# Optimization experiments

Hardware: AMD Instinct MI355X
Metric: run time of the kernel (lower is better)

The kernel has to match this reference:

```python
import jax, jax.numpy as jnp
import numpy as np

DIM = 768
HEADS = 12
HEAD_DIM = DIM // HEADS
HIDDEN = int(DIM * 4.0)


def setup_inputs() -> dict:
    key = jax.random.key(0)
    ks = jax.random.split(key, 12)
    s = lambda *shape: 0.02
    inp = {
        "x": jax.random.normal(ks[0], (8, 1024, DIM), dtype=jnp.float32),
        "norm1_g": jnp.ones((DIM,), jnp.float32),
        "norm1_b": jnp.zeros((DIM,), jnp.float32),
        "qkv_w": jax.random.normal(ks[1], (DIM, 3 * DIM), jnp.float32) * 0.02,
        "qkv_b": jnp.zeros((3 * DIM,), jnp.float32),
        "proj_w": jax.random.normal(ks[2], (DIM, DIM), jnp.float32) * 0.02,
        "proj_b": jnp.zeros((DIM,), jnp.float32),
        "norm2_g": jnp.ones((DIM,), jnp.float32),
        "norm2_b": jnp.zeros((DIM,), jnp.float32),
        "fc1_w": jax.random.normal(ks[3], (DIM, HIDDEN), jnp.float32) * 0.02,
        "fc1_b": jnp.zeros((HIDDEN,), jnp.float32),
        "fc2_w": jax.random.normal(ks[4], (HIDDEN, DIM), jnp.float32) * 0.02,
        "fc2_b": jnp.zeros((DIM,), jnp.float32),
    }
    return inp


def _layernorm(x, g, b, eps=1e-5):
    mu = jnp.mean(x, axis=-1, keepdims=True)
    var = jnp.mean(jnp.square(x - mu), axis=-1, keepdims=True)
    return (x - mu) * jax.lax.rsqrt(var + eps) * g + b


def _attention(x, qkv_w, qkv_b, proj_w, proj_b):
    B, N, C = x.shape
    qkv = x @ qkv_w + qkv_b                      # [B, N, 3C]
    qkv = qkv.reshape(B, N, 3, HEADS, HEAD_DIM)
    q, k, v = jnp.moveaxis(qkv, 2, 0)            # each [B, N, H, D]
    scale = HEAD_DIM ** -0.5
    scores = jnp.einsum("bnhd,bmhd->bhnm", q, k) * scale  # [B, H, N, N]
    attn = jax.nn.softmax(scores, axis=-1)
    out = jnp.einsum("bhnm,bmhd->bnhd", attn, v).reshape(B, N, C)
    return out @ proj_w + proj_b


def reference(x, norm1_g, norm1_b, qkv_w, qkv_b, proj_w, proj_b,
              norm2_g, norm2_b, fc1_w, fc1_b, fc2_w, fc2_b):
    # Pre-norm transformer block (inference: DropPath = identity)
    x = x + _attention(_layernorm(x, norm1_g, norm1_b), qkv_w, qkv_b, proj_w, proj_b)
    h = _layernorm(x, norm2_g, norm2_b)
    h = jax.nn.gelu(h @ fc1_w + fc1_b, approximate=False) @ fc2_w + fc2_b
    return x + h
```

## Files before the change

### kernel.cpp

```cpp
#include <hip/hip_runtime.h>

typedef __attribute__((ext_vector_type(8))) short s16x8;
typedef __attribute__((ext_vector_type(4))) short s16x4;
typedef __attribute__((ext_vector_type(4))) float f32x4;

static __device__ __forceinline__ short f2bf(float f) {
    unsigned u = __builtin_bit_cast(unsigned, f);
    u = (u + 0x7FFFu + ((u >> 16) & 1u)) >> 16;
    return (short)u;
}

__device__ __forceinline__ void gload16(const short* g, short* l) {
    __builtin_amdgcn_global_load_lds(
        (const __attribute__((address_space(1))) void*)g,
        (__attribute__((address_space(3))) void*)l,
        16, 0, 0);
}

__global__ __launch_bounds__(256) void transpose_convert(
    const float* __restrict__ W, short* __restrict__ Wt, int K, int N)
{
    __shared__ float tile[32][33];
    const int bx = blockIdx.x * 32;
    const int by = blockIdx.y * 32;
    const int tx = threadIdx.x;
    const int ty = threadIdx.y;
    for (int i = 0; i < 32; i += 8)
        tile[ty + i][tx] = W[(size_t)(by + ty + i) * N + bx + tx];
    __syncthreads();
    for (int i = 0; i < 32; i += 8)
        Wt[(size_t)(bx + ty + i) * K + by + tx] = f2bf(tile[tx][ty + i]);
}

__global__ __launch_bounds__(256) void layernorm_kernel(
    const float* __restrict__ x, const float* __restrict__ g,
    const float* __restrict__ b, short* __restrict__ out)
{
    const int row = blockIdx.x;
    const float* xr = x + (size_t)row * 768;
    const int t = threadIdx.x;
    float v0 = xr[t], v1 = xr[t + 256], v2 = xr[t + 512];
    __shared__ float red[4];

    float s = v0 + v1 + v2;
    for (int off = 32; off >= 1; off >>= 1) s += __shfl_down(s, off, 64);
    if ((t & 63) == 0) red[t >> 6] = s;
    __syncthreads();
    const float mean = (red[0] + red[1] + red[2] + red[3]) * (1.0f / 768.0f);
    const float d0 = v0 - mean, d1 = v1 - mean, d2 = v2 - mean;
    __syncthreads();
    float ss = d0 * d0 + d1 * d1 + d2 * d2;
    for (int off = 32; off >= 1; off >>= 1) ss += __shfl_down(ss, off, 64);
    if ((t & 63) == 0) red[t >> 6] = ss;
    __syncthreads();
    const float var = (red[0] + red[1] + red[2] + red[3]) * (1.0f / 768.0f);
    const float rstd = rsqrtf(var + 1e-5f);
    out[(size_t)row * 768 + t]       = f2bf(d0 * rstd * g[t] + b[t]);
    out[(size_t)row * 768 + t + 256] = f2bf(d1 * rstd * g[t + 256] + b[t + 256]);
    out[(size_t)row * 768 + t + 512] = f2bf(d2 * rstd * g[t + 512] + b[t + 512]);
}

template <int MODE>
__global__ __launch_bounds__(256) void gemm_bt(
    const short* __restrict__ A, const short* __restrict__ Bt,
    const float* __restrict__ bias, const float* __restrict__ res,
    void* __restrict__ out, short* __restrict__ vtout, int M, int N, int K)
{
    __shared__ __align__(16) short As[128 * 64];
    __shared__ __align__(16) short Bs[128 * 64];

    const int t = threadIdx.x;
    const int l = t & 63;
    const int w = t >> 6;
    const int wr = (w >> 1) * 64;
    const int wc = (w & 1) * 64;

    const int ncol = N >> 7;
    const int xcd = blockIdx.x & 7;
    const int idx = blockIdx.x >> 3;
    const int tn = (idx % ncol) << 7;
    const int tm = ((idx / ncol) * 8 + xcd) << 7;

    const int srow = l >> 3;
    const int scol = ((l & 7) ^ srow) * 8;
    const int c0 = w * 4;
    const short* aS[4]; const short* bS[4];
#pragma unroll
    for (int c = 0; c < 4; c++) {
        const int row = (c0 + c) * 8 + srow;
        aS[c] = A  + (size_t)(tm + row) * K + scol;
        bS[c] = Bt + (size_t)(tn + row) * K + scol;
    }

    const int fr = l & 15;
    const int g = l >> 4;
    const int sl = fr & 7;

    f32x4 acc[4][4] = {};

    for (int k0 = 0; k0 < K; k0 += 64) {
#pragma unroll
        for (int c = 0; c < 4; c++) {
            gload16(aS[c] + k0, &As[(c0 + c) * 512]);
            gload16(bS[c] + k0, &Bs[(c0 + c) * 512]);
        }
        __syncthreads();

        s16x8 af[4][2], bf[4][2];
#pragma unroll
        for (int m = 0; m < 4; m++) {
            const int rbase = (wr + m * 16 + fr) * 64;
            af[m][0] = *(const s16x8*)&As[rbase + ((g ^ sl) * 8)];
            af[m][1] = *(const s16x8*)&As[rbase + (((4 + g) ^ sl) * 8)];
        }
#pragma unroll
        for (int n = 0; n < 4; n++) {
            const int rbase = (wc + n * 16 + fr) * 64;
            bf[n][0] = *(const s16x8*)&Bs[rbase + ((g ^ sl) * 8)];
            bf[n][1] = *(const s16x8*)&Bs[rbase + (((4 + g) ^ sl) * 8)];
        }
#pragma unroll
        for (int m = 0; m < 4; m++)
#pragma unroll
            for (int n = 0; n < 4; n++) {
                acc[m][n] = __builtin_amdgcn_mfma_f32_16x16x32_bf16(af[m][0], bf[n][0], acc[m][n], 0, 0, 0);
                acc[m][n] = __builtin_amdgcn_mfma_f32_16x16x32_bf16(af[m][1], bf[n][1], acc[m][n], 0, 0, 0);
            }
        __syncthreads();
    }

    const int fq = (l >> 4) * 4;
#pragma unroll
    for (int m = 0; m < 4; m++) {
#pragma unroll
        for (int n = 0; n < 4; n++) {
            const int col = tn + wc + n * 16 + fr;
            const float bv = bias[col];
            if (MODE == 3 && col >= 1536) {
                const int row0 = tm + wr + m * 16 + fq;
                const int bb = row0 >> 10;
                const int nseq = row0 & 1023;
                s16x4 ov;
#pragma unroll
                for (int j = 0; j < 4; j++) ov[j] = f2bf(acc[m][n][j] + bv);
                *(s16x4*)(vtout + (((size_t)(bb * 768 + (col - 1536))) << 10) + nseq) = ov;
            } else {
#pragma unroll
                for (int j = 0; j < 4; j++) {
                    const int row = tm + wr + m * 16 + fq + j;
                    float v = acc[m][n][j] + bv;
                    if (MODE == 2) v = 0.5f * v * (1.0f + erff(v * 0.70710678118f));
                    if (MODE == 1) {
                        ((float*)out)[(size_t)row * N + col] = v + res[(size_t)row * N + col];
                    } else {
                        ((short*)out)[(size_t)row * N + col] = f2bf(v);
                    }
                }
            }
        }
    }
}

__global__ __launch_bounds__(256) void attn_kernel(
    const short* __restrict__ qkv, const short* __restrict__ vTg,
    short* __restrict__ out)
{
    const int bid = blockIdx.x;
    const int x = bid & 7;
    const int i = bid >> 3;
    const int bh = x + 8 * (i % 12);
    const int qt = i / 12;
    const int b = bh / 12, h = bh % 12;

    __shared__ __align__(16) short Ks[2][64 * 64];
    __shared__ __align__(16) short Vs[2][64 * 64];
    __shared__ __align__(16) short Ps[4][32][72];

    const int t = threadIdx.x;
    const int l = t & 63;
    const int w = t >> 6;
    const int lq = l & 15;
    const int g = l >> 4;
    const float kSc = 0.18033688011112042f;

    const int q0 = b * 1024 + qt * 128 + w * 32;

    s16x8 qb[2][2];
#pragma unroll
    for (int r = 0; r < 2; r++) {
        const short* qp = qkv + ((size_t)(q0 + r * 16 + lq)) * 2304 + h * 64 + g * 8;
        qb[r][0] = *(const s16x8*)qp;
        qb[r][1] = *(const s16x8*)(qp + 32);
    }

    const int srow = l >> 3;
    const int scol = ((l & 7) ^ srow) * 8;
    const short* kSrc = qkv + (size_t)(b * 1024 + w * 16 + srow) * 2304 + 768 + h * 64 + scol;
    const short* vSrc = vTg + (size_t)(bh * 64 + w * 16 + srow) * 1024 + scol;

    gload16(kSrc,                         &Ks[0][w * 1024]);
    gload16(kSrc + (size_t)8 * 2304,      &Ks[0][w * 1024 + 512]);
    gload16(vSrc,                         &Vs[0][w * 1024]);
    gload16(vSrc + (size_t)8 * 1024,      &Vs[0][w * 1024 + 512]);
    __syncthreads();

    f32x4 acc[2][4] = {};
    float m_run[2] = {-1e30f, -1e30f};
    float l_run[2] = {0.f, 0.f};

    const int swz = (lq & 7) * 8;

    int cur = 0;
    for (int kt = 0; kt < 16; kt++) {
        if (kt < 15) {
            const short* kS = kSrc + (size_t)(kt + 1) * 64 * 2304;
            const short* vS = vSrc + (kt + 1) * 64;
            gload16(kS,                    &Ks[cur ^ 1][w * 1024]);
            gload16(kS + (size_t)8 * 2304, &Ks[cur ^ 1][w * 1024 + 512]);
            gload16(vS,                    &Vs[cur ^ 1][w * 1024]);
            gload16(vS + (size_t)8 * 1024, &Vs[cur ^ 1][w * 1024 + 512]);
        }

        s16x8 ka[4][2];
#pragma unroll
        for (int n = 0; n < 4; n++) {
            const int rbase = (n * 16 + lq) * 64;
            ka[n][0] = *(const s16x8*)&Ks[cur][rbase + ((g * 8) ^ swz)];
            ka[n][1] = *(const s16x8*)&Ks[cur][rbase + ((32 + g * 8) ^ swz)];
        }

        f32x4 s[2][4];
#pragma unroll
        for (int r = 0; r < 2; r++)
#pragma unroll
            for (int n = 0; n < 4; n++) {
                f32x4 sv = {};
                sv = __builtin_amdgcn_mfma_f32_16x16x32_bf16(ka[n][0], qb[r][0], sv, 0, 0, 0);
                sv = __builtin_amdgcn_mfma_f32_16x16x32_bf16(ka[n][1], qb[r][1], sv, 0, 0, 0);
                s[r][n] = sv;
            }

        s16x8 va[4][2];
#pragma unroll
        for (int dt = 0; dt < 4; dt++) {
            const int rbase = (dt * 16 + lq) * 64;
            va[dt][0] = *(const s16x8*)&Vs[cur][rbase + ((g * 8) ^ swz)];
            va[dt][1] = *(const s16x8*)&Vs[cur][rbase + ((32 + g * 8) ^ swz)];
        }

#pragma unroll
        for (int r = 0; r < 2; r++) {
            float mx = fmaxf(fmaxf(s[r][0][0], s[r][0][1]), fmaxf(s[r][0][2], s[r][0][3]));
#pragma unroll
            for (int n = 1; n < 4; n++)
                mx = fmaxf(mx, fmaxf(fmaxf(s[r][n][0], s[r][n][1]), fmaxf(s[r][n][2], s[r][n][3])));
            const float mxs = mx * kSc;
            if (!__all(mxs - m_run[r] <= 8.0f)) {
                float gm = mxs;
                gm = fmaxf(gm, __shfl_xor(gm, 16, 64));
                gm = fmaxf(gm, __shfl_xor(gm, 32, 64));
                const float mnew = fmaxf(m_run[r], gm);
                const float alpha = __builtin_amdgcn_exp2f(m_run[r] - mnew);
                m_run[r] = mnew;
                l_run[r] *= alpha;
#pragma unroll
                for (int dt = 0; dt < 4; dt++) {
                    acc[r][dt][0] *= alpha; acc[r][dt][1] *= alpha;
                    acc[r][dt][2] *= alpha; acc[r][dt][3] *= alpha;
                }
            }
            const float mb = m_run[r];
            float ssum = 0.f;
#pragma unroll
            for (int n = 0; n < 4; n++) {
                const float p0 = __builtin_amdgcn_exp2f(s[r][n][0] * kSc - mb);
                const float p1 = __builtin_amdgcn_exp2f(s[r][n][1] * kSc - mb);
                const float p2 = __builtin_amdgcn_exp2f(s[r][n][2] * kSc - mb);
                const float p3 = __builtin_amdgcn_exp2f(s[r][n][3] * kSc - mb);
                ssum += (p0 + p1) + (p2 + p3);
                unsigned lo, hi;
                asm("v_cvt_pk_bf16_f32 %0, %1, %2" : "=v"(lo) : "v"(p0), "v"(p1));
                asm("v_cvt_pk_bf16_f32 %0, %1, %2" : "=v"(hi) : "v"(p2), "v"(p3));
                unsigned* pp = (unsigned*)&Ps[w][r * 16 + lq][n * 16 + g * 4];
                pp[0] = lo; pp[1] = hi;
            }
            l_run[r] += ssum;
        }

#pragma unroll
        for (int r = 0; r < 2; r++) {
            const s16x8 pb0 = *(const s16x8*)&Ps[w][r * 16 + lq][g * 8];
            const s16x8 pb1 = *(const s16x8*)&Ps[w][r * 16 + lq][32 + g * 8];
#pragma unroll
            for (int dt = 0; dt < 4; dt++) {
                acc[r][dt] = __builtin_amdgcn_mfma_f32_16x16x32_bf16(va[dt][0], pb0, acc[r][dt], 0, 0, 0);
                acc[r][dt] = __builtin_amdgcn_mfma_f32_16x16x32_bf16(va[dt][1], pb1, acc[r][dt], 0, 0, 0);
            }
        }

        __syncthreads();
        if (kt < 15) cur ^= 1;
    }

#pragma unroll
    for (int r = 0; r < 2; r++) {
        float ls = l_run[r];
        ls += __shfl_xor(ls, 16, 64);
        ls += __shfl_xor(ls, 32, 64);
        const float rinv = 1.0f / ls;
        const int qrow = q0 + r * 16 + lq;
#pragma unroll
        for (int dt = 0; dt < 4; dt++) {
            s16x4 ov;
#pragma unroll
            for (int j = 0; j < 4; j++) ov[j] = f2bf(acc[r][dt][j] * rinv);
            *(s16x4*)(out + (size_t)qrow * 768 + h * 64 + dt * 16 + g * 4) = ov;
        }
    }
}

extern "C" void kernel_launch(void* const* d_in, const int* in_sizes, int n_in,
                              void* d_out, int out_size, void* d_ws, size_t ws_size,
                              hipStream_t stream) {
    const float* x      = (const float*)d_in[0];
    const float* n1g    = (const float*)d_in[1];
    const float* n1b    = (const float*)d_in[2];
    const float* qkv_w  = (const float*)d_in[3];
    const float* qkv_b  = (const float*)d_in[4];
    const float* proj_w = (const float*)d_in[5];
    const float* proj_b = (const float*)d_in[6];
    const float* n2g    = (const float*)d_in[7];
    const float* n2b    = (const float*)d_in[8];
    const float* fc1_w  = (const float*)d_in[9];
    const float* fc1_b  = (const float*)d_in[10];
    const float* fc2_w  = (const float*)d_in[11];
    const float* fc2_b  = (const float*)d_in[12];
    float* out = (float*)d_out;

    char* ws = (char*)d_ws;
    short* qkv_wT  = (short*)(ws + 0);
    short* proj_wT = (short*)(ws + 3538944);
    short* fc1_wT  = (short*)(ws + 4718592);
    short* fc2_wT  = (short*)(ws + 9437184);
    short* bufA    = (short*)(ws + 14155776);
    short* bufB    = (short*)(ws + 26738688);
    short* vT      = (short*)(ws + 64487424);
    float* bufC    = (float*)(ws + 77070336);

    const dim3 tb(32, 8);
    transpose_convert<<<dim3(2304 / 32, 768 / 32), tb, 0, stream>>>(qkv_w, qkv_wT, 768, 2304);
    transpose_convert<<<dim3(768 / 32, 768 / 32),  tb, 0, stream>>>(proj_w, proj_wT, 768, 768);
    transpose_convert<<<dim3(3072 / 32, 768 / 32), tb, 0, stream>>>(fc1_w, fc1_wT, 768, 3072);
    transpose_convert<<<dim3(768 / 32, 3072 / 32), tb, 0, stream>>>(fc2_w, fc2_wT, 3072, 768);

    layernorm_kernel<<<8192, 256, 0, stream>>>(x, n1g, n1b, bufA);

    gemm_bt<3><<<64 * (2304 / 128), 256, 0, stream>>>(
        bufA, qkv_wT, qkv_b, nullptr, bufB, vT, 8192, 2304, 768);

    attn_kernel<<<768, 256, 0, stream>>>(bufB, vT, bufA);

    gemm_bt<1><<<64 * (768 / 128), 256, 0, stream>>>(
        bufA, proj_wT, proj_b, x, bufC, nullptr, 8192, 768, 768);

    layernorm_kernel<<<8192, 256, 0, stream>>>(bufC, n2g, n2b, bufA);

    gemm_bt<2><<<64 * (3072 / 128), 256, 0, stream>>>(
        bufA, fc1_wT, fc1_b, nullptr, bufB, nullptr, 8192, 3072, 768);

    gemm_bt<1><<<64 * (768 / 128), 256, 0, stream>>>(
        bufB, fc2_wT, fc2_b, bufC, out, nullptr, 8192, 768, 3072);
}
```

Measured before the change: 279.9 us.

## Add double-buffered 128x64 GEMM for N=768 residual GEMMs, tanh GELU, restructured attention loop

Adds a new gemm_bt_db kernel with 128x64 tiles and two LDS buffers, so the next K-slice loads while the current one is computed. The proj and fc2 GEMMs (N=768) now use it, which also doubles their block count to improve occupancy. The fc1 GELU changes from erff to a tanh approximation built from exp2 and rcp, which cuts transcendental cost but departs from the exact-erf reference. The attention loop is unrolled by two with separate named buffers in place of a runtime index; its schedule stays the same.

After: 244.9 us. -12.5%, faster.

```diff
diff --git a/kernel.cpp b/kernel.cpp
--- a/kernel.cpp
+++ b/kernel.cpp
@@ -83,13 +83,11 @@
 
     const int srow = l >> 3;
     const int scol = ((l & 7) ^ srow) * 8;
-    const int c0 = w * 4;
     const short* aS[4]; const short* bS[4];
 #pragma unroll
     for (int c = 0; c < 4; c++) {
-        const int row = (c0 + c) * 8 + srow;
-        aS[c] = A  + (size_t)(tm + row) * K + scol;
-        bS[c] = Bt + (size_t)(tn + row) * K + scol;
+        aS[c] = A  + (size_t)(tm + (w * 4 + c) * 8 + srow) * K + scol;
+        bS[c] = Bt + (size_t)(tn + (w * 4 + c) * 8 + srow) * K + scol;
     }
 
     const int fr = l & 15;
@@ -101,8 +99,8 @@
     for (int k0 = 0; k0 < K; k0 += 64) {
 #pragma unroll
         for (int c = 0; c < 4; c++) {
-            gload16(aS[c] + k0, &As[(c0 + c) * 512]);
-            gload16(bS[c] + k0, &Bs[(c0 + c) * 512]);
+            gload16(aS[c] + k0, &As[(w * 4 + c) * 512]);
+            gload16(bS[c] + k0, &Bs[(w * 4 + c) * 512]);
         }
         __syncthreads();
 
@@ -149,17 +147,190 @@
                 for (int j = 0; j < 4; j++) {
                     const int row = tm + wr + m * 16 + fq + j;
                     float v = acc[m][n][j] + bv;
-                    if (MODE == 2) v = 0.5f * v * (1.0f + erff(v * 0.70710678118f));
-                    if (MODE == 1) {
-                        ((float*)out)[(size_t)row * N + col] = v + res[(size_t)row * N + col];
-                    } else {
-                        ((short*)out)[(size_t)row * N + col] = f2bf(v);
+                    if (MODE == 2) {
+                        const float u = v * (0.7978845608f + 0.0356774081f * v * v);
+                        const float e = __builtin_amdgcn_exp2f(u * 2.8853900817779268f);
+                        v = v - v * __builtin_amdgcn_rcpf(e + 1.0f);
                     }
+                    ((short*)out)[(size_t)row * N + col] = f2bf(v);
                 }
             }
         }
     }
 }
+
+#define G_STAGE(AS, BS)                                                     \
+    {                                                                       \
+        _Pragma("unroll") for (int c = 0; c < 4; c++) {                     \
+            gload16(aP[c], &AS[(w * 4 + c) * 512]); aP[c] += 64;            \
+        }                                                                   \
+        _Pragma("unroll") for (int c = 0; c < 2; c++) {                     \
+            gload16(bP[c], &BS[(w * 2 + c) * 512]); bP[c] += 64;            \
+        }                                                                   \
+    }
+
+#define G_COMPUTE(AS, BS)                                                   \
+    {                                                                       \
+        s16x8 af[4][2], bf[2][2];                                           \
+        _Pragma("unroll") for (int m = 0; m < 4; m++) {                     \
+            const int rbase = (wr + m * 16 + fr) * 64;                      \
+            af[m][0] = *(const s16x8*)&AS[rbase + ((g ^ sl) * 8)];          \
+            af[m][1] = *(const s16x8*)&AS[rbase + (((4 + g) ^ sl) * 8)];    \
+        }                                                                   \
+        _Pragma("unroll") for (int n = 0; n < 2; n++) {                     \
+            const int rbase = (wc + n * 16 + fr) * 64;                      \
+            bf[n][0] = *(const s16x8*)&BS[rbase + ((g ^ sl) * 8)];          \
+            bf[n][1] = *(const s16x8*)&BS[rbase + (((4 + g) ^ sl) * 8)];    \
+        }                                                                   \
+        _Pragma("unroll") for (int m = 0; m < 4; m++)                       \
+            _Pragma("unroll") for (int n = 0; n < 2; n++) {                 \
+                acc[m][n] = __builtin_amdgcn_mfma_f32_16x16x32_bf16(af[m][0], bf[n][0], acc[m][n], 0, 0, 0); \
+                acc[m][n] = __builtin_amdgcn_mfma_f32_16x16x32_bf16(af[m][1], bf[n][1], acc[m][n], 0, 0, 0); \
+            }                                                               \
+    }
+
+__global__ __launch_bounds__(256) void gemm_bt_db(
+    const short* __restrict__ A, const short* __restrict__ Bt,
+    const float* __restrict__ bias, const float* __restrict__ res,
+    float* __restrict__ out, int M, int N, int K)
+{
+    __shared__ __align__(16) short As0[128 * 64];
+    __shared__ __align__(16) short As1[128 * 64];
+    __shared__ __align__(16) short Bs0[64 * 64];
+    __shared__ __align__(16) short Bs1[64 * 64];
+
+    const int t = threadIdx.x;
+    const int l = t & 63;
+    const int w = t >> 6;
+    const int wr = (w >> 1) * 64;
+    const int wc = (w & 1) * 32;
+
+    const int ncol = N >> 6;
+    const int xcd = blockIdx.x & 7;
+    const int idx = blockIdx.x >> 3;
+    const int tn = (idx % ncol) << 6;
+    const int tm = ((idx / ncol) * 8 + xcd) << 7;
+
+    const int srow = l >> 3;
+    const int scol = ((l & 7) ^ srow) * 8;
+    const short* aP[4]; const short* bP[2];
+#pragma unroll
+    for (int c = 0; c < 4; c++)
+        aP[c] = A  + (size_t)(tm + (w * 4 + c) * 8 + srow) * K + scol;
+#pragma unroll
+    for (int c = 0; c < 2; c++)
+        bP[c] = Bt + (size_t)(tn + (w * 2 + c) * 8 + srow) * K + scol;
+
+    const int fr = l & 15;
+    const int g = l >> 4;
+    const int sl = fr & 7;
+
+    f32x4 acc[4][2] = {};
+
+    G_STAGE(As0, Bs0);
+    __syncthreads();
+
+    const int half = K >> 7;
+    for (int it = 0; it < half; ++it) {
+        G_STAGE(As1, Bs1);
+        G_COMPUTE(As0, Bs0);
+        __syncthreads();
+        if (it < half - 1) G_STAGE(As0, Bs0);
+        G_COMPUTE(As1, Bs1);
+        __syncthreads();
+    }
+
+    const int fq = g * 4;
+#pragma unroll
+    for (int m = 0; m < 4; m++) {
+#pragma unroll
+        for (int n = 0; n < 2; n++) {
+            const int col = tn + wc + n * 16 + fr;
+            const float bv = bias[col];
+#pragma unroll
+            for (int j = 0; j < 4; j++) {
+                const int row = tm + wr + m * 16 + fq + j;
+                out[(size_t)row * N + col] = acc[m][n][j] + bv + res[(size_t)row * N + col];
+            }
+        }
+    }
+}
+
+#define ATTN_STAGE(KS, VS)                                                  \
+    {                                                                       \
+        gload16(kP,                    &KS[w * 1024]);                      \
+        gload16(kP + (size_t)8 * 2304, &KS[w * 1024 + 512]);                \
+        gload16(vP,                    &VS[w * 1024]);                      \
+        gload16(vP + (size_t)8 * 1024, &VS[w * 1024 + 512]);                \
+        kP += (size_t)64 * 2304;                                            \
+        vP += 64;                                                           \
+    }
+
+#define ATTN_COMPUTE(KS, VS)                                                \
+    {                                                                       \
+        s16x8 ka[4][2];                                                     \
+        _Pragma("unroll") for (int n = 0; n < 4; n++) {                     \
+            const int rbase = (n * 16 + lq) * 64;                           \
+            ka[n][0] = *(const s16x8*)&KS[rbase + ((g * 8) ^ swz)];         \
+            ka[n][1] = *(const s16x8*)&KS[rbase + ((32 + g * 8) ^ swz)];    \
+        }                                                                   \
+        f32x4 s[2][4];                                                      \
+        _Pragma("unroll") for (int r = 0; r < 2; r++)                       \
+            _Pragma("unroll") for (int n = 0; n < 4; n++) {                 \
+                f32x4 sv = {};                                              \
+                sv = __builtin_amdgcn_mfma_f32_16x16x32_bf16(ka[n][0], qb[r][0], sv, 0, 0, 0); \
+                sv = __builtin_amdgcn_mfma_f32_16x16x32_bf16(ka[n][1], qb[r][1], sv, 0, 0, 0); \
+                s[r][n] = sv;                                               \
+            }                                                               \
+        s16x8 va[4][2];                                                     \
+        _Pragma("unroll") for (int dt = 0; dt < 4; dt++) {                  \
+            const int rbase = (dt * 16 + lq) * 64;                          \
+            va[dt][0] = *(const s16x8*)&VS[rbase + ((g * 8) ^ swz)];        \
+            va[dt][1] = *(const s16x8*)&VS[rbase + ((32 + g * 8) ^ swz)];   \
+        }                                                                   \
+        _Pragma("unroll") for (int r = 0; r < 2; r++) {                     \
+            float mx = fmaxf(fmaxf(s[r][0][0], s[r][0][1]), fmaxf(s[r][0][2], s[r][0][3])); \
+            _Pragma("unroll") for (int n = 1; n < 4; n++)                   \
+                mx = fmaxf(mx, fmaxf(fmaxf(s[r][n][0], s[r][n][1]), fmaxf(s[r][n][2], s[r][n][3]))); \
+            const float mxs = mx * kSc;                                     \
+            if (!__all(mxs - m_run[r] <= 8.0f)) {                           \
+                float gm = mxs;                                             \
+                gm = fmaxf(gm, __shfl_xor(gm, 16, 64));                     \
+                gm = fmaxf(gm, __shfl_xor(gm, 32, 64));                     \
+                const float mnew = fmaxf(m_run[r], gm);                     \
+                const float alpha = __builtin_amdgcn_exp2f(m_run[r] - mnew);\
+                m_run[r] = mnew;                                            \
+                l_run[r] *= alpha;                                          \
+                _Pragma("unroll") for (int dt = 0; dt < 4; dt++) {          \
+                    acc[r][dt][0] *= alpha; acc[r][dt][1] *= alpha;         \
+                    acc[r][dt][2] *= alpha; acc[r][dt][3] *= alpha;         \
+                }                                                           \
+            }                                                               \
+            const float mb = m_run[r];                                      \
+            float ssum = 0.f;                                               \
+            _Pragma("unroll") for (int n = 0; n < 4; n++) {                 \
+                const float p0 = __builtin_amdgcn_exp2f(s[r][n][0] * kSc - mb); \
+                const float p1 = __builtin_amdgcn_exp2f(s[r][n][1] * kSc - mb); \
+                const float p2 = __builtin_amdgcn_exp2f(s[r][n][2] * kSc - mb); \
+                const float p3 = __builtin_amdgcn_exp2f(s[r][n][3] * kSc - mb); \
+                ssum += (p0 + p1) + (p2 + p3);                              \
+                unsigned lo, hi;                                            \
+                asm("v_cvt_pk_bf16_f32 %0, %1, %2" : "=v"(lo) : "v"(p0), "v"(p1)); \
+                asm("v_cvt_pk_bf16_f32 %0, %1, %2" : "=v"(hi) : "v"(p2), "v"(p3)); \
+                unsigned* pp = (unsigned*)&Ps[w][r * 16 + lq][n * 16 + g * 4]; \
+                pp[0] = lo; pp[1] = hi;                                     \
+            }                                                               \
+            l_run[r] += ssum;                                               \
+        }                                                                   \
+        _Pragma("unroll") for (int r = 0; r < 2; r++) {                     \
+            const s16x8 pb0 = *(const s16x8*)&Ps[w][r * 16 + lq][g * 8];    \
+            const s16x8 pb1 = *(const s16x8*)&Ps[w][r * 16 + lq][32 + g * 8]; \
+            _Pragma("unroll") for (int dt = 0; dt < 4; dt++) {              \
+                acc[r][dt] = __builtin_amdgcn_mfma_f32_16x16x32_bf16(va[dt][0], pb0, acc[r][dt], 0, 0, 0); \
+                acc[r][dt] = __builtin_amdgcn_mfma_f32_16x16x32_bf16(va[dt][1], pb1, acc[r][dt], 0, 0, 0); \
+            }                                                               \
+        }                                                                   \
+    }
 
 __global__ __launch_bounds__(256) void attn_kernel(
     const short* __restrict__ qkv, const short* __restrict__ vTg,
@@ -172,8 +343,10 @@
     const int qt = i / 12;
     const int b = bh / 12, h = bh % 12;
 
-    __shared__ __align__(16) short Ks[2][64 * 64];
-    __shared__ __align__(16) short Vs[2][64 * 64];
+    __shared__ __align__(16) short Ks0[64 * 64];
+    __shared__ __align__(16) short Ks1[64 * 64];
+    __shared__ __align__(16) short Vs0[64 * 64];
+    __shared__ __align__(16) short Vs1[64 * 64];
     __shared__ __align__(16) short Ps[4][32][72];
 
     const int t = threadIdx.x;
@@ -195,14 +368,8 @@
 
     const int srow = l >> 3;
     const int scol = ((l & 7) ^ srow) * 8;
-    const short* kSrc = qkv + (size_t)(b * 1024 + w * 16 + srow) * 2304 + 768 + h * 64 + scol;
-    const short* vSrc = vTg + (size_t)(bh * 64 + w * 16 + srow) * 1024 + scol;
-
-    gload16(kSrc,                         &Ks[0][w * 1024]);
-    gload16(kSrc + (size_t)8 * 2304,      &Ks[0][w * 1024 + 512]);
-    gload16(vSrc,                         &Vs[0][w * 1024]);
-    gload16(vSrc + (size_t)8 * 1024,      &Vs[0][w * 1024 + 512]);
-    __syncthreads();
+    const short* kP = qkv + (size_t)(b * 1024 + w * 16 + srow) * 2304 + 768 + h * 64 + scol;
+    const short* vP = vTg + (size_t)(bh * 64 + w * 16 + srow) * 1024 + scol;
 
     f32x4 acc[2][4] = {};
     float m_run[2] = {-1e30f, -1e30f};
@@ -210,96 +377,16 @@
 
     const int swz = (lq & 7) * 8;
 
-    int cur = 0;
-    for (int kt = 0; kt < 16; kt++) {
-        if (kt < 15) {
-            const short* kS = kSrc + (size_t)(kt + 1) * 64 * 2304;
-            const short* vS = vSrc + (kt + 1) * 64;
-            gload16(kS,                    &Ks[cur ^ 1][w * 1024]);
-            gload16(kS + (size_t)8 * 2304, &Ks[cur ^ 1][w * 1024 + 512]);
-            gload16(vS,                    &Vs[cur ^ 1][w * 1024]);
-            gload16(vS + (size_t)8 * 1024, &Vs[cur ^ 1][w * 1024 + 512]);
-        }
-
-        s16x8 ka[4][2];
-#pragma unroll
-        for (int n = 0; n < 4; n++) {
-            const int rbase = (n * 16 + lq) * 64;
-            ka[n][0] = *(const s16x8*)&Ks[cur][rbase + ((g * 8) ^ swz)];
-            ka[n][1] = *(const s16x8*)&Ks[cur][rbase + ((32 + g * 8) ^ swz)];
-        }
-
-        f32x4 s[2][4];
-#pragma unroll
-        for (int r = 0; r < 2; r++)
-#pragma unroll
-            for (int n = 0; n < 4; n++) {
-                f32x4 sv = {};
-                sv = __builtin_amdgcn_mfma_f32_16x16x32_bf16(ka[n][0], qb[r][0], sv, 0, 0, 0);
-                sv = __builtin_amdgcn_mfma_f32_16x16x32_bf16(ka[n][1], qb[r][1], sv, 0, 0, 0);
-                s[r][n] = sv;
-            }
-
-        s16x8 va[4][2];
-#pragma unroll
-        for (int dt = 0; dt < 4; dt++) {
-            const int rbase = (dt * 16 + lq) * 64;
-            va[dt][0] = *(const s16x8*)&Vs[cur][rbase + ((g * 8) ^ swz)];
-            va[dt][1] = *(const s16x8*)&Vs[cur][rbase + ((32 + g * 8) ^ swz)];
-        }
-
-#pragma unroll
-        for (int r = 0; r < 2; r++) {
-            float mx = fmaxf(fmaxf(s[r][0][0], s[r][0][1]), fmaxf(s[r][0][2], s[r][0][3]));
-#pragma unroll
-            for (int n = 1; n < 4; n++)
-                mx = fmaxf(mx, fmaxf(fmaxf(s[r][n][0], s[r][n][1]), fmaxf(s[r][n][2], s[r][n][3])));
-            const float mxs = mx * kSc;
-            if (!__all(mxs - m_run[r] <= 8.0f)) {
-                float gm = mxs;
-                gm = fmaxf(gm, __shfl_xor(gm, 16, 64));
-                gm = fmaxf(gm, __shfl_xor(gm, 32, 64));
-                const float mnew = fmaxf(m_run[r], gm);
-                const float alpha = __builtin_amdgcn_exp2f(m_run[r] - mnew);
-                m_run[r] = mnew;
-                l_run[r] *= alpha;
-#pragma unroll
-                for (int dt = 0; dt < 4; dt++) {
-                    acc[r][dt][0] *= alpha; acc[r][dt][1] *= alpha;
-                    acc[r][dt][2] *= alpha; acc[r][dt][3] *= alpha;
-                }
-            }
-            const float mb = m_run[r];
-            float ssum = 0.f;
-#pragma unroll
-            for (int n = 0; n < 4; n++) {
-                const float p0 = __builtin_amdgcn_exp2f(s[r][n][0] * kSc - mb);
-                const float p1 = __builtin_amdgcn_exp2f(s[r][n][1] * kSc - mb);
-                const float p2 = __builtin_amdgcn_exp2f(s[r][n][2] * kSc - mb);
-                const float p3 = __builtin_amdgcn_exp2f(s[r][n][3] * kSc - mb);
-                ssum += (p0 + p1) + (p2 + p3);
-                unsigned lo, hi;
-                asm("v_cvt_pk_bf16_f32 %0, %1, %2" : "=v"(lo) : "v"(p0), "v"(p1));
-                asm("v_cvt_pk_bf16_f32 %0, %1, %2" : "=v"(hi) : "v"(p2), "v"(p3));
-                unsigned* pp = (unsigned*)&Ps[w][r * 16 + lq][n * 16 + g * 4];
-                pp[0] = lo; pp[1] = hi;
-            }
-            l_run[r] += ssum;
-        }
-
-#pragma unroll
-        for (int r = 0; r < 2; r++) {
-            const s16x8 pb0 = *(const s16x8*)&Ps[w][r * 16 + lq][g * 8];
-            const s16x8 pb1 = *(const s16x8*)&Ps[w][r * 16 + lq][32 + g * 8];
-#pragma unroll
-            for (int dt = 0; dt < 4; dt++) {
-                acc[r][dt] = __builtin_amdgcn_mfma_f32_16x16x32_bf16(va[dt][0], pb0, acc[r][dt], 0, 0, 0);
-                acc[r][dt] = __builtin_amdgcn_mfma_f32_16x16x32_bf16(va[dt][1], pb1, acc[r][dt], 0, 0, 0);
-            }
-        }
-
-        __syncthreads();
-        if (kt < 15) cur ^= 1;
+    ATTN_STAGE(Ks0, Vs0);
+    __syncthreads();
+
+    for (int it = 0; it < 8; ++it) {
+        ATTN_STAGE(Ks1, Vs1);
+        ATTN_COMPUTE(Ks0, Vs0);
+        __syncthreads();
+        if (it < 7) ATTN_STAGE(Ks0, Vs0);
+        ATTN_COMPUTE(Ks1, Vs1);
+        __syncthreads();
     }
 
 #pragma unroll
@@ -360,14 +447,14 @@
 
     attn_kernel<<<768, 256, 0, stream>>>(bufB, vT, bufA);
 
-    gemm_bt<1><<<64 * (768 / 128), 256, 0, stream>>>(
-        bufA, proj_wT, proj_b, x, bufC, nullptr, 8192, 768, 768);
+    gemm_bt_db<<<64 * (768 / 64), 256, 0, stream>>>(
+        bufA, proj_wT, proj_b, x, bufC, 8192, 768, 768);
 
     layernorm_kernel<<<8192, 256, 0, stream>>>(bufC, n2g, n2b, bufA);
 
     gemm_bt<2><<<64 * (3072 / 128), 256, 0, stream>>>(
         bufA, fc1_wT, fc1_b, nullptr, bufB, nullptr, 8192, 3072, 768);
 
-    gemm_bt<1><<<64 * (768 / 128), 256, 0, stream>>>(
-        bufB, fc2_wT, fc2_b, bufC, out, nullptr, 8192, 768, 3072);
-}
+    gemm_bt_db<<<64 * (768 / 64), 256, 0, stream>>>(
+        bufB, fc2_wT, fc2_b, bufC, out, 8192, 768, 3072);
+}
```
